# Performance work log

Measured on AMD Instinct MI355X. Metric: run time of the kernel, lower is better.

## Reference

```python
import math
import jax, jax.numpy as jnp
import numpy as np

B, T, C = 2, 2048, 2048
H, G = 16, 4
D = C // H  # head_dim = 128
KV = G * D
SOFT_CAP = 50.0
EPS = 1e-6


def setup_inputs() -> dict:
    key = jax.random.key(0)
    ks = jax.random.split(key, 5)
    s = 1.0 / math.sqrt(C)
    return {
        "x": jax.random.normal(ks[0], (B, T, C), jnp.float32),
        "Wq": jax.random.normal(ks[1], (C, C), jnp.float32) * s,
        "Wk": jax.random.normal(ks[2], (KV, C), jnp.float32) * s,
        "Wv": jax.random.normal(ks[3], (KV, C), jnp.float32) * s,
        "Wo": jax.random.normal(ks[4], (C, C), jnp.float32) * s,
        "bo": jnp.zeros((C,), jnp.float32),
        "q_norm_w": jnp.ones((D,), jnp.float32),
        "k_norm_w": jnp.ones((D,), jnp.float32),
    }


def _rmsnorm(x, w):
    # norm/sqrt(d) formulation, eps added to rms (matches torch module exactly)
    rms = jnp.linalg.norm(x, axis=-1, keepdims=True) / math.sqrt(x.shape[-1])
    return w * (x / (rms + EPS))


def _rotary_tables(seq_len, dim):
    inv_freq = 1.0 / (10000.0 ** (jnp.arange(0, dim, 2, dtype=jnp.float32) / dim))
    t = jnp.arange(seq_len, dtype=jnp.float32)
    freqs = jnp.outer(t, inv_freq)  # [T, D/2]
    return jnp.cos(freqs), jnp.sin(freqs)


def _apply_rope(x, cos, sin):
    # x: [B, T, h, D]; cos/sin: [T, D/2] broadcast as [1, T, 1, D/2]
    d = x.shape[-1] // 2
    x1, x2 = x[..., :d], x[..., d:]
    c = cos[None, :, None, :]
    s = sin[None, :, None, :]
    return jnp.concatenate([x1 * c + x2 * s, -x1 * s + x2 * c], axis=-1)


def reference(x, Wq, Wk, Wv, Wo, bo, q_norm_w, k_norm_w):
    b, t, c = x.shape
    q = (x @ Wq.T).reshape(b, t, H, D)
    k = (x @ Wk.T).reshape(b, t, G, D)
    v = (x @ Wv.T).reshape(b, t, G, D)

    cos, sin = _rotary_tables(t, D)
    q = _apply_rope(_rmsnorm(q, q_norm_w), cos, sin)
    k = _apply_rope(_rmsnorm(k, k_norm_w), cos, sin)

    q = q.transpose(0, 2, 1, 3)              # [B, H, T, D]
    k = jnp.repeat(k.transpose(0, 2, 1, 3), H // G, axis=1)  # [B, H, T, D]
    v = jnp.repeat(v.transpose(0, 2, 1, 3), H // G, axis=1)

    att = jnp.einsum("bhqd,bhkd->bhqk", q, k) / math.sqrt(D)
    causal = jnp.tril(jnp.ones((t, t), bool))
    att = jnp.where(causal[None, None], att, -jnp.inf)
    att = SOFT_CAP * jnp.tanh(att / SOFT_CAP)  # masked entries -> -50
    att = jax.nn.softmax(att, axis=-1)

    y = jnp.einsum("bhqk,bhkd->bhqd", att, v)
    y = y.transpose(0, 2, 1, 3).reshape(b, t, c)
    return y @ Wo.T + bo
```

## Files before the change

kernel.cpp:

```cpp
#include <hip/hip_runtime.h>
#include <math.h>

#define T_SEQ 2048
#define C_DIM 2048
#define NH    16
#define NG    4
#define DH    128
#define BATCH 2

typedef unsigned short u16;
typedef unsigned long long u64;
typedef __bf16 bf16_t;
typedef bf16_t bf16x8 __attribute__((ext_vector_type(8)));
typedef float  f32x4  __attribute__((ext_vector_type(4)));

static __device__ __forceinline__ u16 f2bf(float f) {
    return __builtin_bit_cast(u16, (__bf16)f);
}

static __device__ __forceinline__ void gll16(const void* g, void* lds) {
    __builtin_amdgcn_global_load_lds(
        (const __attribute__((address_space(1))) void*)(unsigned long long)(g),
        (__attribute__((address_space(3))) void*)(unsigned int)(unsigned long long)(lds),
        16, 0, 0);
}

__global__ __launch_bounds__(256)
void cast_multi(const float* __restrict__ x,  const float* __restrict__ wq,
                const float* __restrict__ wk, const float* __restrict__ wv,
                const float* __restrict__ wo,
                u16* __restrict__ xo, u16* __restrict__ wqo,
                u16* __restrict__ wko, u16* __restrict__ wvo,
                u16* __restrict__ woo) {
    int i = blockIdx.x * 256 + threadIdx.x;
    const float* src; u16* dst; int off;
    if (i < 1048576)      { src = x;  dst = xo;  off = i; }
    else if (i < 1572864) { src = wq; dst = wqo; off = i - 1048576; }
    else if (i < 1703936) { src = wk; dst = wko; off = i - 1572864; }
    else if (i < 1835008) { src = wv; dst = wvo; off = i - 1703936; }
    else                  { src = wo; dst = woo; off = i - 1835008; }
    const float4* p = (const float4*)src + (size_t)off * 2;
    float4 a = p[0], b = p[1];
    u16 u[8] = {f2bf(a.x), f2bf(a.y), f2bf(a.z), f2bf(a.w),
                f2bf(b.x), f2bf(b.y), f2bf(b.z), f2bf(b.w)};
    *(uint4*)(dst + (size_t)off * 8) = *(const uint4*)u;
}

__global__ __launch_bounds__(256)
void rope_tables(float* __restrict__ cosT, float* __restrict__ sinT) {
    int i = blockIdx.x * 256 + threadIdx.x;
    int tp = i >> 6, ln = i & 63;
    float invfreq = __builtin_amdgcn_exp2f(-(float)ln * (13.287712379549449f / 64.0f));
    float s, c;
    sincosf((float)tp * invfreq, &s, &c);
    cosT[i] = c;
    sinT[i] = s;
}

static __device__ __forceinline__ void gemm_core(
        u16* As, u16* Bs,
        const u16* __restrict__ A, const u16* __restrict__ B,
        int K, int m0, int n0, f32x4 (&acc)[4][4]) {
    const int t    = threadIdx.x;
    const int lane = t & 63, w = t >> 6;
    const int l15  = lane & 15, quad = lane >> 4;
    const int wr   = w >> 1, wc = w & 1;

#pragma unroll
    for (int mt = 0; mt < 4; ++mt)
#pragma unroll
        for (int nt = 0; nt < 4; ++nt) acc[mt][nt] = (f32x4){0.f, 0.f, 0.f, 0.f};

    const int off0 = w*2048 + lane*16;
    const int r0 = off0 >> 6,          c0 = (off0 & 63) >> 1;
    const int r1 = (off0+1024) >> 6,   c1 = ((off0+1024) & 63) >> 1;
    const u16* Ag0 = A + (size_t)(m0 + r0) * K + c0;
    const u16* Ag1 = A + (size_t)(m0 + r1) * K + c1;
    const u16* Bg0 = B + (size_t)(n0 + r0) * K + c0;
    const u16* Bg1 = B + (size_t)(n0 + r1) * K + c1;
    char* AsB = (char*)As; char* BsB = (char*)Bs;
    const int ldsOff0 = w*2048, ldsOff1 = w*2048 + 1024;

    for (int k0 = 0; k0 < K; k0 += 32) {
        gll16(Ag0 + k0, AsB + ldsOff0);
        gll16(Ag1 + k0, AsB + ldsOff1);
        gll16(Bg0 + k0, BsB + ldsOff0);
        gll16(Bg1 + k0, BsB + ldsOff1);
        __syncthreads();
        bf16x8 af[4], bf[4];
#pragma unroll
        for (int mt = 0; mt < 4; ++mt)
            af[mt] = __builtin_bit_cast(bf16x8,
                *(const uint4*)&As[(wr*64 + mt*16 + l15)*32 + quad*8]);
#pragma unroll
        for (int nt = 0; nt < 4; ++nt)
            bf[nt] = __builtin_bit_cast(bf16x8,
                *(const uint4*)&Bs[(wc*64 + nt*16 + l15)*32 + quad*8]);
#pragma unroll
        for (int mt = 0; mt < 4; ++mt)
#pragma unroll
            for (int nt = 0; nt < 4; ++nt)
                acc[mt][nt] = __builtin_amdgcn_mfma_f32_16x16x32_bf16(
                                  af[mt], bf[nt], acc[mt][nt], 0, 0, 0);
        __syncthreads();
    }
}

__global__ __launch_bounds__(256)
void gemm_nt_bf16(const u16* __restrict__ A, const u16* __restrict__ B,
                  const float* __restrict__ bias, float* __restrict__ C,
                  int N, int K) {
    __shared__ __align__(16) u16 As[128*32];
    __shared__ __align__(16) u16 Bs[128*32];
    const int m0 = blockIdx.y*128, n0 = blockIdx.x*128;
    f32x4 acc[4][4];
    gemm_core(As, Bs, A, B, K, m0, n0, acc);

    const int t    = threadIdx.x;
    const int lane = t & 63, w = t >> 6;
    const int l15  = lane & 15, quad = lane >> 4;
    const int wr   = w >> 1, wc = w & 1;
#pragma unroll
    for (int mt = 0; mt < 4; ++mt)
#pragma unroll
        for (int nt = 0; nt < 4; ++nt) {
            const int col = n0 + wc*64 + nt*16 + l15;
            const float bv = bias ? bias[col] : 0.f;
#pragma unroll
            for (int r = 0; r < 4; ++r) {
                const int row = m0 + wr*64 + mt*16 + quad*4 + r;
                C[(size_t)row * N + col] = acc[mt][nt][r] + bv;
            }
        }
}

__global__ __launch_bounds__(256)
void gemm_qkv(const u16* __restrict__ A,  const u16* __restrict__ Bq,
              const u16* __restrict__ Bk, const u16* __restrict__ Bv,
              float* __restrict__ Cq, float* __restrict__ Ck,
              u16* __restrict__ vt) {
    __shared__ __align__(16) u16 As[128*32];
    __shared__ __align__(16) u16 Bs[128*32];
    const int bx = blockIdx.x;
    const u16* B; int N, n0, mode;
    if (bx < 16)      { B = Bq; N = 2048; n0 = bx * 128;      mode = 0; }
    else if (bx < 20) { B = Bk; N = 512;  n0 = (bx-16) * 128; mode = 1; }
    else              { B = Bv; N = 512;  n0 = (bx-20) * 128; mode = 2; }
    const int m0 = blockIdx.y * 128;

    f32x4 acc[4][4];
    gemm_core(As, Bs, A, B, 2048, m0, n0, acc);

    const int t    = threadIdx.x;
    const int lane = t & 63, w = t >> 6;
    const int l15  = lane & 15, quad = lane >> 4;
    const int wr   = w >> 1, wc = w & 1;

    if (mode == 2) {
        const int g  = bx - 20;
        const int bb = m0 >> 11;
        const int tb = (m0 & (T_SEQ - 1)) + wr*64 + quad*4;
#pragma unroll
        for (int mt = 0; mt < 4; ++mt) {
            const int tpos = tb + mt*16;
#pragma unroll
            for (int nt = 0; nt < 4; ++nt) {
                const int d = wc*64 + nt*16 + l15;
                u16 pk[4] = {f2bf(acc[mt][nt][0]), f2bf(acc[mt][nt][1]),
                             f2bf(acc[mt][nt][2]), f2bf(acc[mt][nt][3])};
                *(u64*)(vt + ((size_t)((bb*NG + g)*DH + d))*T_SEQ + tpos) =
                    *(const u64*)pk;
            }
        }
        return;
    }

    float* C = mode ? Ck : Cq;
#pragma unroll
    for (int mt = 0; mt < 4; ++mt)
#pragma unroll
        for (int nt = 0; nt < 4; ++nt) {
            const int col = n0 + wc*64 + nt*16 + l15;
#pragma unroll
            for (int r = 0; r < 4; ++r) {
                const int row = m0 + wr*64 + mt*16 + quad*4 + r;
                C[(size_t)row * N + col] = acc[mt][nt][r];
            }
        }
}

__global__ __launch_bounds__(256)
void rmsnorm_rope_qk(const float* __restrict__ qf, const float* __restrict__ kf,
                     const float* __restrict__ qw, const float* __restrict__ kw,
                     const float* __restrict__ cosT, const float* __restrict__ sinT,
                     u16* __restrict__ qo, u16* __restrict__ ko) {
    const int blk  = blockIdx.x;
    const int sub  = threadIdx.x >> 6;
    const int lane = threadIdx.x & 63;
    const float* in; const float* w; u16* out; int row, nheads; float scale;
    if (blk < 16384) {
        in = qf; w = qw; out = qo; nheads = NH; scale = 0.08838834764831845f;
        row = blk * 4 + sub;
    } else {
        in = kf; w = kw; out = ko; nheads = NG; scale = 1.0f;
        row = (blk - 16384) * 4 + sub;
    }
    const float* p = in + (size_t)row * 128;
    float x1 = p[lane], x2 = p[lane + 64];
    float ss = x1*x1 + x2*x2;
#pragma unroll
    for (int off = 32; off >= 1; off >>= 1) ss += __shfl_xor(ss, off, 64);
    float inv = 1.0f / (sqrtf(ss * (1.0f/128.0f)) + 1e-6f);
    float x1n = w[lane]      * x1 * inv;
    float x2n = w[lane + 64] * x2 * inv;
    int tpos = (row / nheads) & (T_SEQ - 1);
    float c = cosT[tpos*64 + lane];
    float s = sinT[tpos*64 + lane];
    out[(size_t)row*128 + lane]      = f2bf((x1n * c + x2n * s) * scale);
    out[(size_t)row*128 + lane + 64] = f2bf((x2n * c - x1n * s) * scale);
}

__global__ __launch_bounds__(256, 2)
void flash_attn_mfma(const u16* __restrict__ qh, const u16* __restrict__ kh,
                     const u16* __restrict__ vt, u16* __restrict__ y) {
    __shared__ __align__(16) u16 Ks[2][64*128];
    __shared__ __align__(16) u16 Vs[2][128*64];

    const int t    = threadIdx.x;
    const int lane = t & 63, w = t >> 6;
    const int l15  = lane & 15, quad = lane >> 4;
    const int bg   = blockIdx.y;
    const int b    = bg >> 2, g = bg & 3;
    const int chunk = b ? (int)blockIdx.x : (63 - (int)blockIdx.x);
    const int q0   = chunk * 32;
    const int h    = g * (NH / NG) + w;

    const float C0 =  1.4426950408889634f;
    const float C1 = -0.48089834696298777f;
    const float C2 =  0.19235933878519512f;
    const float C3 = -0.07785972536301652f;

    bf16x8 aq[2][4];
#pragma unroll
    for (int m = 0; m < 2; ++m) {
        const u16* qp = qh + ((size_t)(b*T_SEQ + q0 + m*16 + l15) * NH + h) * DH;
#pragma unroll
        for (int kc = 0; kc < 4; ++kc)
            aq[m][kc] = __builtin_bit_cast(bf16x8, *(const uint4*)(qp + kc*32 + quad*8));
    }

    f32x4 accO[2][8];
#pragma unroll
    for (int m = 0; m < 2; ++m)
#pragma unroll
        for (int nd = 0; nd < 8; ++nd) accO[m][nd] = (f32x4){0.f, 0.f, 0.f, 0.f};
    float ls[2] = {0.f, 0.f};

    const u16* kgb = kh + ((size_t)b*T_SEQ*NG + g)*DH;
    const u16* vgb = vt + ((size_t)(b*NG + g)*DH)*T_SEQ;

    const int krb = t >> 4, kcl = t & 15;
    const int vdb = t >> 3, vcl = t & 7;

    const int ktiles = q0/64 + 1;

#pragma unroll
    for (int j = 0; j < 4; ++j) {
        const int kr = j*16 + krb;
        const int rp = kr & 31;
        const int kphys = (kr & 32) + ((rp >> 2) & 3)*8 + (rp >> 4)*4 + (rp & 3);
        gll16(kgb + (size_t)kphys*(NG*DH) + ((kcl ^ (kr & 7)) << 3),
              (char*)Ks[0] + j*4096 + w*1024);
        const int vd = j*32 + vdb;
        gll16(vgb + (size_t)vd*T_SEQ + ((vcl ^ (vd & 7)) << 3),
              (char*)Vs[0] + j*4096 + w*1024);
    }

    for (int kt = 0; kt < ktiles; ++kt) {
        asm volatile("s_waitcnt vmcnt(0)" ::: "memory");
        __syncthreads();

        if (kt + 1 < ktiles) {
            const int k0n = (kt + 1) * 64, bn = (kt + 1) & 1;
#pragma unroll
            for (int j = 0; j < 4; ++j) {
                const int kr = j*16 + krb;
                const int rp = kr & 31;
                const int kphys = (kr & 32) + ((rp >> 2) & 3)*8 + (rp >> 4)*4 + (rp & 3);
                gll16(kgb + (size_t)(k0n + kphys)*(NG*DH) + ((kcl ^ (kr & 7)) << 3),
                      (char*)Ks[bn] + j*4096 + w*1024);
                const int vd = j*32 + vdb;
                gll16(vgb + (size_t)vd*T_SEQ + k0n + ((vcl ^ (vd & 7)) << 3),
                      (char*)Vs[bn] + j*4096 + w*1024);
            }
        }

        const u16* Kb = Ks[kt & 1];
        const u16* Vb = Vs[kt & 1];
        const int k0 = kt * 64;
        const bool diag = (kt == ktiles - 1);

        bf16x8 pa[2][2];
#pragma unroll
        for (int b32 = 0; b32 < 2; ++b32) {
            alignas(16) u16 pk0[8];
            alignas(16) u16 pk1[8];
#pragma unroll
            for (int sub = 0; sub < 2; ++sub) {
                const int kc16 = b32*2 + sub;
                const int krow = kc16*16 + l15;
                const int kswz = (krow & 7) << 3;
                f32x4 st0 = (f32x4){0.f,0.f,0.f,0.f};
                f32x4 st1 = (f32x4){0.f,0.f,0.f,0.f};
#pragma unroll
                for (int kc = 0; kc < 4; ++kc) {
                    bf16x8 ak = __builtin_bit_cast(bf16x8,
                        *(const uint4*)&Kb[krow*128 + ((kc*32 + quad*8) ^ kswz)]);
                    st0 = __builtin_amdgcn_mfma_f32_16x16x32_bf16(ak, aq[0][kc], st0, 0, 0, 0);
                    st1 = __builtin_amdgcn_mfma_f32_16x16x32_bf16(ak, aq[1][kc], st1, 0, 0, 0);
                }
#pragma unroll
                for (int m = 0; m < 2; ++m) {
                    const f32x4 st = m ? st1 : st0;
#pragma unroll
                    for (int r = 0; r < 4; ++r) {
                        float sv = st[r];
                        float z = sv * 0.02f;
                        float u = z * z;
                        float poly = fmaf(u, fmaf(u, fmaf(u, C3, C2), C1), C0);
                        float pv = __builtin_amdgcn_exp2f(sv * poly);
                        if (diag) {
                            const int keyg = k0 + b32*32 + quad*8 + sub*4 + r;
                            const int qg   = q0 + m*16 + l15;
                            pv = (keyg > qg) ? 0.f : pv;
                        }
                        ls[m] += pv;
                        if (m) pk1[sub*4 + r] = f2bf(pv);
                        else   pk0[sub*4 + r] = f2bf(pv);
                    }
                }
            }
            pa[0][b32] = __builtin_bit_cast(bf16x8, *(const uint4*)pk0);
            pa[1][b32] = __builtin_bit_cast(bf16x8, *(const uint4*)pk1);
        }

#pragma unroll
        for (int nd = 0; nd < 8; ++nd) {
            const int vrow = nd*16 + l15;
            const int vswz = (vrow & 7) << 3;
#pragma unroll
            for (int b32 = 0; b32 < 2; ++b32) {
                bf16x8 bv = __builtin_bit_cast(bf16x8,
                    *(const uint4*)&Vb[vrow*64 + ((b32*32 + quad*8) ^ vswz)]);
                accO[0][nd] = __builtin_amdgcn_mfma_f32_16x16x32_bf16(pa[0][b32], bv, accO[0][nd], 0, 0, 0);
                accO[1][nd] = __builtin_amdgcn_mfma_f32_16x16x32_bf16(pa[1][b32], bv, accO[1][nd], 0, 0, 0);
            }
        }
    }

#pragma unroll
    for (int m = 0; m < 2; ++m) {
        float v = ls[m];
        v += __shfl_xor(v, 16, 64);
        v += __shfl_xor(v, 32, 64);
        ls[m] = v;
    }

#pragma unroll
    for (int m = 0; m < 2; ++m)
#pragma unroll
        for (int r = 0; r < 4; ++r) {
            const float invl = 1.f / __shfl(ls[m], quad*4 + r, 64);
            u16* yp = y + (size_t)(b*T_SEQ + q0 + m*16 + quad*4 + r) * C_DIM + h*DH;
#pragma unroll
            for (int nd = 0; nd < 8; ++nd)
                yp[nd*16 + l15] = f2bf(accO[m][nd][r] * invl);
        }
}

extern "C" void kernel_launch(void* const* d_in, const int* in_sizes, int n_in,
                              void* d_out, int out_size, void* d_ws, size_t ws_size,
                              hipStream_t stream) {
    const float* x  = (const float*)d_in[0];
    const float* Wq = (const float*)d_in[1];
    const float* Wk = (const float*)d_in[2];
    const float* Wv = (const float*)d_in[3];
    const float* Wo = (const float*)d_in[4];
    const float* bo = (const float*)d_in[5];
    const float* qw = (const float*)d_in[6];
    const float* kw = (const float*)d_in[7];
    float* out = (float*)d_out;

    const size_t qE = (size_t)BATCH * T_SEQ * NH * DH;
    const size_t kE = (size_t)BATCH * T_SEQ * NG * DH;
    const size_t wqE = (size_t)C_DIM * C_DIM;
    const size_t wkE = (size_t)(NG*DH) * C_DIM;

    float* qf  = (float*)d_ws;
    float* kf  = qf + qE;
    u16*   qh  = (u16*)(kf + kE);
    u16*   khb = qh + qE;
    u16*   vtb = khb + kE;
    u16*   xh  = vtb + kE;
    u16*   wqh = xh + qE;
    u16*   wkh = wqh + wqE;
    u16*   wvh = wkh + wkE;
    u16*   woh = wvh + wkE;
    float* cosT = (float*)(woh + wqE);
    float* sinT = cosT + 131072;
    u16*   yh  = (u16*)qf;

    const int M = BATCH * T_SEQ;
    dim3 blk(256);

    rope_tables<<<dim3(512), blk, 0, stream>>>(cosT, sinT);

    cast_multi<<<dim3(9216), blk, 0, stream>>>(x, Wq, Wk, Wv, Wo,
                                               xh, wqh, wkh, wvh, woh);

    gemm_qkv<<<dim3(24, M/128), blk, 0, stream>>>(xh, wqh, wkh, wvh,
                                                  qf, kf, vtb);

    rmsnorm_rope_qk<<<dim3(M*NH/4 + M*NG/4), blk, 0, stream>>>(qf, kf, qw, kw, cosT, sinT, qh, khb);

    flash_attn_mfma<<<dim3(T_SEQ/32, BATCH*NG), blk, 0, stream>>>(qh, khb, vtb, yh);

    gemm_nt_bf16<<<dim3(C_DIM/128, M/128), blk, 0, stream>>>(yh, woh, bo, out, C_DIM, C_DIM);
}
```

Before: 348.7 us.

## Merge prep kernels and move V transpose into an LDS-staged norm kernel

Combines the bf16 cast and rope-table kernels into one launch. The QKV GEMM now writes V row-major in bf16 instead of scattered 8-byte transposed stores. A tiled transpose through LDS, appended as extra blocks of the RMSNorm/RoPE kernel, then produces the transposed V layout. This trades uncoalesced GEMM epilogue stores and one kernel launch for an extra V round trip through memory and added LDS use in the norm kernel.

New measurement: 351.0 us. Within noise of the previous version (+0.7%).

```diff
diff --git a/kernel.cpp b/kernel.cpp
--- a/kernel.cpp
+++ b/kernel.cpp
@@ -26,35 +26,36 @@
 }
 
 __global__ __launch_bounds__(256)
-void cast_multi(const float* __restrict__ x,  const float* __restrict__ wq,
-                const float* __restrict__ wk, const float* __restrict__ wv,
-                const float* __restrict__ wo,
-                u16* __restrict__ xo, u16* __restrict__ wqo,
-                u16* __restrict__ wko, u16* __restrict__ wvo,
-                u16* __restrict__ woo) {
-    int i = blockIdx.x * 256 + threadIdx.x;
-    const float* src; u16* dst; int off;
-    if (i < 1048576)      { src = x;  dst = xo;  off = i; }
-    else if (i < 1572864) { src = wq; dst = wqo; off = i - 1048576; }
-    else if (i < 1703936) { src = wk; dst = wko; off = i - 1572864; }
-    else if (i < 1835008) { src = wv; dst = wvo; off = i - 1703936; }
-    else                  { src = wo; dst = woo; off = i - 1835008; }
-    const float4* p = (const float4*)src + (size_t)off * 2;
-    float4 a = p[0], b = p[1];
-    u16 u[8] = {f2bf(a.x), f2bf(a.y), f2bf(a.z), f2bf(a.w),
-                f2bf(b.x), f2bf(b.y), f2bf(b.z), f2bf(b.w)};
-    *(uint4*)(dst + (size_t)off * 8) = *(const uint4*)u;
-}
-
-__global__ __launch_bounds__(256)
-void rope_tables(float* __restrict__ cosT, float* __restrict__ sinT) {
-    int i = blockIdx.x * 256 + threadIdx.x;
-    int tp = i >> 6, ln = i & 63;
-    float invfreq = __builtin_amdgcn_exp2f(-(float)ln * (13.287712379549449f / 64.0f));
-    float s, c;
-    sincosf((float)tp * invfreq, &s, &c);
-    cosT[i] = c;
-    sinT[i] = s;
+void prep(const float* __restrict__ x,  const float* __restrict__ wq,
+          const float* __restrict__ wk, const float* __restrict__ wv,
+          const float* __restrict__ wo,
+          u16* __restrict__ xo, u16* __restrict__ wqo,
+          u16* __restrict__ wko, u16* __restrict__ wvo,
+          u16* __restrict__ woo,
+          float* __restrict__ cosT, float* __restrict__ sinT) {
+    const int bid = blockIdx.x;
+    if (bid < 9216) {
+        int i = bid * 256 + threadIdx.x;
+        const float* src; u16* dst; int off;
+        if (i < 1048576)      { src = x;  dst = xo;  off = i; }
+        else if (i < 1572864) { src = wq; dst = wqo; off = i - 1048576; }
+        else if (i < 1703936) { src = wk; dst = wko; off = i - 1572864; }
+        else if (i < 1835008) { src = wv; dst = wvo; off = i - 1703936; }
+        else                  { src = wo; dst = woo; off = i - 1835008; }
+        const float4* p = (const float4*)src + (size_t)off * 2;
+        float4 a = p[0], b = p[1];
+        u16 u[8] = {f2bf(a.x), f2bf(a.y), f2bf(a.z), f2bf(a.w),
+                    f2bf(b.x), f2bf(b.y), f2bf(b.z), f2bf(b.w)};
+        *(uint4*)(dst + (size_t)off * 8) = *(const uint4*)u;
+    } else {
+        int i = (bid - 9216) * 256 + threadIdx.x;
+        int tp = i >> 6, ln = i & 63;
+        float invfreq = __builtin_amdgcn_exp2f(-(float)ln * (13.287712379549449f / 64.0f));
+        float s, c;
+        sincosf((float)tp * invfreq, &s, &c);
+        cosT[i] = c;
+        sinT[i] = s;
+    }
 }
 
 static __device__ __forceinline__ void gemm_core(
@@ -138,7 +139,7 @@
 void gemm_qkv(const u16* __restrict__ A,  const u16* __restrict__ Bq,
               const u16* __restrict__ Bk, const u16* __restrict__ Bv,
               float* __restrict__ Cq, float* __restrict__ Ck,
-              u16* __restrict__ vt) {
+              u16* __restrict__ vfh) {
     __shared__ __align__(16) u16 As[128*32];
     __shared__ __align__(16) u16 Bs[128*32];
     const int bx = blockIdx.x;
@@ -157,21 +158,17 @@
     const int wr   = w >> 1, wc = w & 1;
 
     if (mode == 2) {
-        const int g  = bx - 20;
-        const int bb = m0 >> 11;
-        const int tb = (m0 & (T_SEQ - 1)) + wr*64 + quad*4;
-#pragma unroll
-        for (int mt = 0; mt < 4; ++mt) {
-            const int tpos = tb + mt*16;
+#pragma unroll
+        for (int mt = 0; mt < 4; ++mt)
 #pragma unroll
             for (int nt = 0; nt < 4; ++nt) {
-                const int d = wc*64 + nt*16 + l15;
-                u16 pk[4] = {f2bf(acc[mt][nt][0]), f2bf(acc[mt][nt][1]),
-                             f2bf(acc[mt][nt][2]), f2bf(acc[mt][nt][3])};
-                *(u64*)(vt + ((size_t)((bb*NG + g)*DH + d))*T_SEQ + tpos) =
-                    *(const u64*)pk;
-            }
-        }
+                const int col = n0 + wc*64 + nt*16 + l15;
+#pragma unroll
+                for (int r = 0; r < 4; ++r) {
+                    const int row = m0 + wr*64 + mt*16 + quad*4 + r;
+                    vfh[(size_t)row * 512 + col] = f2bf(acc[mt][nt][r]);
+                }
+            }
         return;
     }
 
@@ -190,34 +187,70 @@
 }
 
 __global__ __launch_bounds__(256)
-void rmsnorm_rope_qk(const float* __restrict__ qf, const float* __restrict__ kf,
-                     const float* __restrict__ qw, const float* __restrict__ kw,
-                     const float* __restrict__ cosT, const float* __restrict__ sinT,
-                     u16* __restrict__ qo, u16* __restrict__ ko) {
-    const int blk  = blockIdx.x;
-    const int sub  = threadIdx.x >> 6;
-    const int lane = threadIdx.x & 63;
-    const float* in; const float* w; u16* out; int row, nheads; float scale;
-    if (blk < 16384) {
-        in = qf; w = qw; out = qo; nheads = NH; scale = 0.08838834764831845f;
-        row = blk * 4 + sub;
-    } else {
-        in = kf; w = kw; out = ko; nheads = NG; scale = 1.0f;
-        row = (blk - 16384) * 4 + sub;
-    }
-    const float* p = in + (size_t)row * 128;
-    float x1 = p[lane], x2 = p[lane + 64];
-    float ss = x1*x1 + x2*x2;
-#pragma unroll
-    for (int off = 32; off >= 1; off >>= 1) ss += __shfl_xor(ss, off, 64);
-    float inv = 1.0f / (sqrtf(ss * (1.0f/128.0f)) + 1e-6f);
-    float x1n = w[lane]      * x1 * inv;
-    float x2n = w[lane + 64] * x2 * inv;
-    int tpos = (row / nheads) & (T_SEQ - 1);
-    float c = cosT[tpos*64 + lane];
-    float s = sinT[tpos*64 + lane];
-    out[(size_t)row*128 + lane]      = f2bf((x1n * c + x2n * s) * scale);
-    out[(size_t)row*128 + lane + 64] = f2bf((x2n * c - x1n * s) * scale);
+void norm_qk_vt(const float* __restrict__ qf, const float* __restrict__ kf,
+                const float* __restrict__ qw, const float* __restrict__ kw,
+                const float* __restrict__ cosT, const float* __restrict__ sinT,
+                const u16* __restrict__ vfh,
+                u16* __restrict__ qo, u16* __restrict__ ko, u16* __restrict__ vt) {
+    __shared__ u16 Lt[128 * 66];
+    const int blk = blockIdx.x;
+    const int t   = threadIdx.x;
+
+    if (blk < 20480) {
+        const int sub  = t >> 6;
+        const int lane = t & 63;
+        const float* in; const float* w; u16* out; int row, nheads; float scale;
+        if (blk < 16384) {
+            in = qf; w = qw; out = qo; nheads = NH; scale = 0.08838834764831845f;
+            row = blk * 4 + sub;
+        } else {
+            in = kf; w = kw; out = ko; nheads = NG; scale = 1.0f;
+            row = (blk - 16384) * 4 + sub;
+        }
+        const float* p = in + (size_t)row * 128;
+        float x1 = p[lane], x2 = p[lane + 64];
+        float ss = x1*x1 + x2*x2;
+#pragma unroll
+        for (int off = 32; off >= 1; off >>= 1) ss += __shfl_xor(ss, off, 64);
+        float inv = 1.0f / (sqrtf(ss * (1.0f/128.0f)) + 1e-6f);
+        float x1n = w[lane]      * x1 * inv;
+        float x2n = w[lane + 64] * x2 * inv;
+        int tpos = (row / nheads) & (T_SEQ - 1);
+        float c = cosT[tpos*64 + lane];
+        float s = sinT[tpos*64 + lane];
+        out[(size_t)row*128 + lane]      = f2bf((x1n * c + x2n * s) * scale);
+        out[(size_t)row*128 + lane + 64] = f2bf((x2n * c - x1n * s) * scale);
+        return;
+    }
+
+    const int idx = blk - 20480;
+    const int t0  = (idx & 31) * 64;
+    const int bg  = idx >> 5;
+    const int b   = bg / NG, g = bg % NG;
+#pragma unroll
+    for (int rep = 0; rep < 4; ++rep) {
+        int ii = rep * 256 + t;
+        int i  = ii >> 4;
+        int c  = ii & 15;
+        uint4 vv = *(const uint4*)(vfh + ((size_t)(b*T_SEQ + t0 + i)*NG + g)*DH + c*8);
+        const u16* pv = (const u16*)&vv;
+#pragma unroll
+        for (int jj = 0; jj < 8; ++jj)
+            Lt[(c*8 + jj)*66 + i] = pv[jj];
+    }
+    __syncthreads();
+#pragma unroll
+    for (int rep = 0; rep < 4; ++rep) {
+        int ii = rep * 256 + t;
+        int d = ii >> 3, c = ii & 7;
+        const u16* src = &Lt[d*66 + c*8];
+        uint4 val;
+        val.x = *(const unsigned int*)(src + 0);
+        val.y = *(const unsigned int*)(src + 2);
+        val.z = *(const unsigned int*)(src + 4);
+        val.w = *(const unsigned int*)(src + 6);
+        *(uint4*)(vt + ((size_t)(bg*DH + d))*T_SEQ + t0 + c*8) = val;
+    }
 }
 
 __global__ __launch_bounds__(256, 2)
@@ -400,7 +433,8 @@
     float* kf  = qf + qE;
     u16*   qh  = (u16*)(kf + kE);
     u16*   khb = qh + qE;
-    u16*   vtb = khb + kE;
+    u16*   vfh = khb + kE;
+    u16*   vtb = vfh + kE;
     u16*   xh  = vtb + kE;
     u16*   wqh = xh + qE;
     u16*   wkh = wqh + wqE;
@@ -413,15 +447,14 @@
     const int M = BATCH * T_SEQ;
     dim3 blk(256);
 
-    rope_tables<<<dim3(512), blk, 0, stream>>>(cosT, sinT);
-
-    cast_multi<<<dim3(9216), blk, 0, stream>>>(x, Wq, Wk, Wv, Wo,
-                                               xh, wqh, wkh, wvh, woh);
+    prep<<<dim3(9728), blk, 0, stream>>>(x, Wq, Wk, Wv, Wo,
+                                         xh, wqh, wkh, wvh, woh, cosT, sinT);
 
     gemm_qkv<<<dim3(24, M/128), blk, 0, stream>>>(xh, wqh, wkh, wvh,
-                                                  qf, kf, vtb);
-
-    rmsnorm_rope_qk<<<dim3(M*NH/4 + M*NG/4), blk, 0, stream>>>(qf, kf, qw, kw, cosT, sinT, qh, khb);
+                                                  qf, kf, vfh);
+
+    norm_qk_vt<<<dim3(M*NH/4 + M*NG/4 + 256), blk, 0, stream>>>(
+        qf, kf, qw, kw, cosT, sinT, vfh, qh, khb, vtb);
 
     flash_attn_mfma<<<dim3(T_SEQ/32, BATCH*NG), blk, 0, stream>>>(qh, khb, vtb, yh);
 
```
